# Optimization experiments

Hardware: AMD Instinct MI355X
Metric: run time of the kernel (lower is better)

The kernel has to match this reference:

```python
import jax, jax.numpy as jnp
import numpy as np

WH, WW = 7, 7
N = WH * WW
HEADS = 12
HEAD_DIM = 16
EMBED = 384
INNER = HEADS * HEAD_DIM
NW = 64
B_ = 2048
SCALE = HEAD_DIM ** -0.5


def _relative_position_index():
    ch, cw = np.meshgrid(np.arange(WH), np.arange(WW), indexing='ij')
    coords = np.stack([ch.ravel(), cw.ravel()])              # [2, N]
    rel = coords[:, :, None] - coords[:, None, :]             # [2, N, N]
    rel = rel.transpose(1, 2, 0)
    rel[:, :, 0] += WH - 1
    rel[:, :, 1] += WW - 1
    rel[:, :, 0] *= 2 * WW - 1
    return jnp.asarray(rel.sum(-1), dtype=jnp.int32)          # [N, N]


def setup_inputs() -> dict:
    key = jax.random.key(0)
    ks = jax.random.split(key, 8)
    s_in = EMBED ** -0.5
    s_inner = INNER ** -0.5
    x = jax.random.normal(ks[0], (B_, N, EMBED), jnp.float32)
    # Swin shift mask: 0 or -100 per window pair
    mbits = jax.random.bernoulli(ks[1], 0.2, (NW, N, N))
    mask = jnp.where(mbits, jnp.float32(-100.0), jnp.float32(0.0))
    return {
        'x': x,
        'mask': mask,
        'Wq': jax.random.normal(ks[2], (EMBED, INNER), jnp.float32) * s_in,
        'bq': jnp.zeros((INNER,), jnp.float32),
        'Wk': jax.random.normal(ks[3], (EMBED, INNER), jnp.float32) * s_in,
        'bk': jnp.zeros((INNER,), jnp.float32),
        'Wv': jax.random.normal(ks[4], (EMBED, INNER), jnp.float32) * s_in,
        'bv': jnp.zeros((INNER,), jnp.float32),
        'Wp': jax.random.normal(ks[5], (INNER, EMBED), jnp.float32) * s_inner,
        'bp': jnp.zeros((EMBED,), jnp.float32),
        'bias_table': jax.random.normal(ks[6], ((2 * WH - 1) * (2 * WW - 1), HEADS), jnp.float32) * 0.02,
        'rel_idx': _relative_position_index(),
    }


def reference(x, mask, Wq, bq, Wk, bk, Wv, bv, Wp, bp, bias_table, rel_idx):
    B, n, _ = x.shape
    q = (x @ Wq + bq).reshape(B, n, HEADS, HEAD_DIM)
    k = (x @ Wk + bk).reshape(B, n, HEADS, HEAD_DIM)
    v = (x @ Wv + bv).reshape(B, n, HEADS, HEAD_DIM)
    attn = jnp.einsum('bnhd,bmhd->bhnm', q * SCALE, k)        # [B, H, N, N]
    bias = bias_table[rel_idx]                                 # [N, N, H]
    attn = attn + jnp.transpose(bias, (2, 0, 1))[None]
    nW = mask.shape[0]
    attn = attn.reshape(B // nW, nW, HEADS, n, n) + mask[None, :, None]
    attn = jax.nn.softmax(attn.reshape(B, HEADS, n, n), axis=-1)
    out = jnp.einsum('bhnm,bmhd->bnhd', attn, v).reshape(B, n, INNER)
    return out @ Wp + bp
```

## Files before the change

kernel.cpp:

```cpp
#include <hip/hip_runtime.h>


typedef __attribute__((ext_vector_type(8))) short  bf8;
typedef __attribute__((ext_vector_type(4))) short  bf4;
typedef __attribute__((ext_vector_type(4))) float  f4;

#define L2E 1.4426950408889634f

union VU { unsigned u[2]; bf4 v; };

__device__ __forceinline__ short f2b(float f) {
  unsigned u = __builtin_bit_cast(unsigned, f);
  unsigned r = u + 0x7fffu + ((u >> 16) & 1u);
  return (short)(r >> 16);
}
__device__ __forceinline__ unsigned pk2(float lo, float hi) {
  return (unsigned)(unsigned short)f2b(lo) | ((unsigned)(unsigned short)f2b(hi) << 16);
}
__device__ __forceinline__ bf4 pkbf4(f4 v) {
  VU r; r.u[0] = pk2(v[0], v[1]); r.u[1] = pk2(v[2], v[3]);
  return r.v;
}
__device__ __forceinline__ float b2f(unsigned short b) {
  return __builtin_bit_cast(float, (unsigned)b << 16);
}
__device__ __forceinline__ float ex2(float x) {
#if __has_builtin(__builtin_amdgcn_exp2f)
  return __builtin_amdgcn_exp2f(x);
#else
  float r; asm("v_exp_f32 %0, %1" : "=v"(r) : "v"(x)); return r;
#endif
}
__device__ __forceinline__ f4 mfma16(bf4 a, bf4 b, f4 c) {
#if __has_builtin(__builtin_amdgcn_mfma_f32_16x16x16bf16_1k)
  return __builtin_amdgcn_mfma_f32_16x16x16bf16_1k(a, b, c, 0, 0, 0);
#else
  f4 d;
  asm("v_mfma_f32_16x16x16_bf16 %0, %1, %2, %3" : "=v"(d) : "v"(a), "v"(b), "v"(c));
  return d;
#endif
}

__global__ void wa_prep(const float* __restrict__ Wq, const float* __restrict__ Wk,
                        const float* __restrict__ Wv, const float* __restrict__ Wp,
                        const float* __restrict__ btab, const int* __restrict__ ridx,
                        const float* __restrict__ mask,
                        short* __restrict__ wt, short* __restrict__ wpt,
                        unsigned short* __restrict__ biasS, unsigned short* __restrict__ maskS) {
  int id = blockIdx.x * 256 + threadIdx.x;
  const int NWT = 576 * 384, NWP = 384 * 192, NBS = 12 * 64 * 64, NMS = 64 * 64 * 64;
  if (id < NWT) {
    int row = id / 384, k = id - row * 384;
    int kind = row / 192, cc = row - kind * 192;
    const float* W = (kind == 0) ? Wq : (kind == 1 ? Wk : Wv);
    float v = W[k * 192 + cc];
    if (kind == 0) v *= 0.25f * L2E;
    wt[id] = f2b(v);
  } else if ((id -= NWT) < NWP) {
    int n = id / 192, k = id - n * 192;
    wpt[id] = f2b(Wp[k * 384 + n]);
  } else if ((id -= NWP) < NBS) {
    int h = id >> 12, rem = id & 4095;
    int n = rem >> 6, cc = rem & 63;
    int m = (cc & 3) * 16 + (cc >> 2);
    float v;
    if (n >= 49)      v = -14427.0f;
    else if (m >= 49) v = 0.0f;
    else              v = btab[ridx[m * 49 + n] * 12 + h] * L2E;
    biasS[id] = (unsigned short)f2b(v);
  } else if ((id -= NBS) < NMS) {
    int win = id >> 12, rem = id & 4095;
    int n = rem >> 6, cc = rem & 63;
    int m = (cc & 3) * 16 + (cc >> 2);
    float v = (m < 49 && n < 49) ? mask[win * 2401 + m * 49 + n] * L2E : 0.f;
    maskS[id] = (unsigned short)f2b(v);
  }
}

struct __align__(16) Smem {
  union U {
    short xs[64][392];
    struct QK { short qs[64][200]; short ks[64][200]; } qk;
  } u;
};

__global__ __launch_bounds__(256, 2)
void wa_main(const float* __restrict__ x,
             const float* __restrict__ bq, const float* __restrict__ bk,
             const float* __restrict__ bv, const float* __restrict__ bp,
             const short* __restrict__ wt, const short* __restrict__ wpt,
             const unsigned short* __restrict__ biasS, const unsigned short* __restrict__ maskS,
             float* __restrict__ out) {
  __shared__ Smem sm;
  const int tid = threadIdx.x;
  const int w   = tid >> 6;
  const int lid = tid & 63;
  const int g   = lid >> 4;
  const int c   = lid & 15;
  const int blk = blockIdx.x;
  const int mwin = (blk & 63) << 12;

  {
    const float* xw = x + (size_t)blk * 18816;
    f4 xv[18];
#pragma unroll
    for (int it = 0; it < 18; it++) {
      int i = tid + it * 256;
      xv[it] = *(const f4*)(xw + (i / 96) * 384 + (i % 96) * 4);
    }
    const int iT = tid + 18 * 256;
    f4 xt = {0.f, 0.f, 0.f, 0.f};
    if (iT < 4704) xt = *(const f4*)(xw + (iT / 96) * 384 + (iT % 96) * 4);
#pragma unroll
    for (int it = 0; it < 18; it++) {
      int i = tid + it * 256;
      *(bf4*)&sm.u.xs[i / 96][(i % 96) * 4] = pkbf4(xv[it]);
    }
    if (iT < 4704) *(bf4*)&sm.u.xs[iT / 96][(iT % 96) * 4] = pkbf4(xt);
    const bf8 zz = {0,0,0,0,0,0,0,0};
#pragma unroll
    for (int it = 0; it < 3; it++) {
      int i = tid + it * 256;
      if (i < 735) { int row = 49 + i / 49, c8 = (i % 49) * 8; *(bf8*)&sm.u.xs[row][c8] = zz; }
    }
  }
  __syncthreads();

  f4 acc[4][9];
#pragma unroll
  for (int mt = 0; mt < 4; mt++)
#pragma unroll
    for (int i = 0; i < 9; i++) acc[mt][i] = (f4){0.f, 0.f, 0.f, 0.f};
  int rowb[9];
#pragma unroll
  for (int i = 0; i < 9; i++) {
    int kind = i / 3, hh = 3 * w + i % 3;
    rowb[i] = (kind * 192 + hh * 16 + c) * 384;
  }
#pragma unroll 3
  for (int ks = 0; ks < 12; ks++) {
    const int k0 = ks * 32 + g * 8;
    bf8 a[4], b[9];
#pragma unroll
    for (int mt = 0; mt < 4; mt++) a[mt] = *(const bf8*)&sm.u.xs[mt * 16 + c][k0];
#pragma unroll
    for (int i = 0; i < 9; i++) b[i] = *(const bf8*)(wt + rowb[i] + k0);
#pragma unroll
    for (int mt = 0; mt < 4; mt++)
#pragma unroll
      for (int i = 0; i < 9; i++)
        acc[mt][i] = __builtin_amdgcn_mfma_f32_16x16x32_bf16(a[mt], b[i], acc[mt][i], 0, 0, 0);
  }
  __syncthreads();

  unsigned vpk[3][4][2];
#pragma unroll
  for (int i = 0; i < 9; i++) {
    const int kind = i / 3, hh = 3 * w + i % 3;
    const int col = hh * 16 + c;
    const float bb = (kind == 0) ? (0.25f * L2E) * bq[col] : (kind == 1 ? bk[col] : bv[col]);
#pragma unroll
    for (int mt = 0; mt < 4; mt++) {
      unsigned w0 = pk2(acc[mt][i][0] + bb, acc[mt][i][1] + bb);
      unsigned w1 = pk2(acc[mt][i][2] + bb, acc[mt][i][3] + bb);
      if (kind == 2) {
        vpk[i - 6][mt][0] = w0;
        vpk[i - 6][mt][1] = w1;
      } else {
        short* dst = (kind == 0) ? &sm.u.qk.qs[0][0] : &sm.u.qk.ks[0][0];
        dst[(mt * 16 + g * 4 + 0) * 200 + col] = (short)(w0 & 0xFFFFu);
        dst[(mt * 16 + g * 4 + 1) * 200 + col] = (short)(w0 >> 16);
        dst[(mt * 16 + g * 4 + 2) * 200 + col] = (short)(w1 & 0xFFFFu);
        dst[(mt * 16 + g * 4 + 3) * 200 + col] = (short)(w1 >> 16);
      }
    }
  }
  asm volatile("" ::: "memory");

  const f4 z4 = {0.f, 0.f, 0.f, 0.f};
#pragma unroll
  for (int t = 0; t < 3; t++) {
    const int h  = 3 * w + t;
    const int hb = h * 16;
    bf4 afr[4], bfr[4];
#pragma unroll
    for (int nt = 0; nt < 4; nt++)
      afr[nt] = *(const bf4*)&sm.u.qk.ks[nt * 16 + c][hb + g * 4];
#pragma unroll
    for (int mt = 0; mt < 4; mt++)
      bfr[mt] = *(const bf4*)&sm.u.qk.qs[mt * 16 + c][hb + g * 4];
    f4 s[4][4];
#pragma unroll
    for (int nt = 0; nt < 4; nt++)
#pragma unroll
      for (int mt = 0; mt < 4; mt++)
        s[nt][mt] = mfma16(afr[nt], bfr[mt], z4);
    const unsigned short* bsH = biasS + (h << 12);
#pragma unroll
    for (int nt = 0; nt < 4; nt++)
#pragma unroll
      for (int r = 0; r < 4; r++) {
        const int n = nt * 16 + g * 4 + r;
        bf4 b4 = *(const bf4*)&bsH[n * 64 + c * 4];
        bf4 m4 = *(const bf4*)&maskS[mwin + n * 64 + c * 4];
#pragma unroll
        for (int mt = 0; mt < 4; mt++)
          s[nt][mt][r] += b2f((unsigned short)b4[mt]) + b2f((unsigned short)m4[mt]);
      }
    float rin[4];
#pragma unroll
    for (int mt = 0; mt < 4; mt++) {
      float mx = -3e38f;
#pragma unroll
      for (int nt = 0; nt < 4; nt++)
#pragma unroll
        for (int r = 0; r < 4; r++) mx = fmaxf(mx, s[nt][mt][r]);
      mx = fmaxf(mx, __shfl_xor(mx, 16, 64));
      mx = fmaxf(mx, __shfl_xor(mx, 32, 64));
      float sum = 0.f;
#pragma unroll
      for (int nt = 0; nt < 4; nt++)
#pragma unroll
        for (int r = 0; r < 4; r++) {
          float p = ex2(s[nt][mt][r] - mx);
          s[nt][mt][r] = p;
          sum += p;
        }
      sum += __shfl_xor(sum, 16, 64);
      sum += __shfl_xor(sum, 32, 64);
      rin[mt] = 1.f / sum;
    }
    unsigned ppk[4][4][2];
#pragma unroll
    for (int nt = 0; nt < 4; nt++)
#pragma unroll
      for (int mt = 0; mt < 4; mt++) {
        ppk[nt][mt][0] = pk2(s[nt][mt][0], s[nt][mt][1]);
        ppk[nt][mt][1] = pk2(s[nt][mt][2], s[nt][mt][3]);
      }
    f4 o[4];
#pragma unroll
    for (int mt = 0; mt < 4; mt++) o[mt] = z4;
#pragma unroll
    for (int kt = 0; kt < 4; kt++) {
      VU vu; vu.u[0] = vpk[t][kt][0]; vu.u[1] = vpk[t][kt][1];
#pragma unroll
      for (int mt = 0; mt < 4; mt++) {
        VU pu; pu.u[0] = ppk[kt][mt][0]; pu.u[1] = ppk[kt][mt][1];
        o[mt] = mfma16(vu.v, pu.v, o[mt]);
      }
    }
#pragma unroll
    for (int mt = 0; mt < 4; mt++) {
      f4 ov = o[mt] * rin[mt];
      *(bf4*)&sm.u.qk.qs[mt * 16 + c][hb + g * 4] = pkbf4(ov);
    }
    asm volatile("" ::: "memory");
  }

  bf8 wb0[6];
#pragma unroll
  for (int jt = 0; jt < 6; jt++)
    wb0[jt] = *(const bf8*)(wpt + (w * 96 + jt * 16 + c) * 192 + g * 8);
  __syncthreads();

  f4 acc3[6][4];
#pragma unroll
  for (int jt = 0; jt < 6; jt++)
#pragma unroll
    for (int mt = 0; mt < 4; mt++) acc3[jt][mt] = z4;
  {
    const int k0 = g * 8;
    bf8 ao[4];
#pragma unroll
    for (int mt = 0; mt < 4; mt++) ao[mt] = *(const bf8*)&sm.u.qk.qs[mt * 16 + c][k0];
#pragma unroll
    for (int jt = 0; jt < 6; jt++)
#pragma unroll
      for (int mt = 0; mt < 4; mt++)
        acc3[jt][mt] = __builtin_amdgcn_mfma_f32_16x16x32_bf16(wb0[jt], ao[mt], acc3[jt][mt], 0, 0, 0);
  }
#pragma unroll 2
  for (int ks3 = 1; ks3 < 6; ks3++) {
    const int k0 = ks3 * 32 + g * 8;
    bf8 ao[4], wb[6];
#pragma unroll
    for (int mt = 0; mt < 4; mt++) ao[mt] = *(const bf8*)&sm.u.qk.qs[mt * 16 + c][k0];
#pragma unroll
    for (int jt = 0; jt < 6; jt++)
      wb[jt] = *(const bf8*)(wpt + (w * 96 + jt * 16 + c) * 192 + k0);
#pragma unroll
    for (int jt = 0; jt < 6; jt++)
#pragma unroll
      for (int mt = 0; mt < 4; mt++)
        acc3[jt][mt] = __builtin_amdgcn_mfma_f32_16x16x32_bf16(wb[jt], ao[mt], acc3[jt][mt], 0, 0, 0);
  }
  float* ow = out + (size_t)blk * 18816;
#pragma unroll
  for (int jt = 0; jt < 6; jt++) {
    const int colb = w * 96 + jt * 16 + g * 4;
    const f4 bp4 = *(const f4*)&bp[colb];
#pragma unroll
    for (int mt = 0; mt < 4; mt++) {
      const int m = mt * 16 + c;
      if (m < 49) {
        f4 v = acc3[jt][mt] + bp4;
        *(f4*)&ow[m * 384 + colb] = v;
      }
    }
  }
}

extern "C" void kernel_launch(void* const* d_in, const int* in_sizes, int n_in,
                              void* d_out, int out_size, void* d_ws, size_t ws_size,
                              hipStream_t stream) {
  const float* x    = (const float*)d_in[0];
  const float* mask = (const float*)d_in[1];
  const float* Wq   = (const float*)d_in[2];
  const float* bq   = (const float*)d_in[3];
  const float* Wk   = (const float*)d_in[4];
  const float* bk   = (const float*)d_in[5];
  const float* Wv   = (const float*)d_in[6];
  const float* bv   = (const float*)d_in[7];
  const float* Wp   = (const float*)d_in[8];
  const float* bp   = (const float*)d_in[9];
  const float* btab = (const float*)d_in[10];
  const int*   ridx = (const int*)d_in[11];
  float* out = (float*)d_out;

  char* ws = (char*)d_ws;
  short* wt            = (short*)ws;
  short* wpt           = (short*)(ws + 442368);
  unsigned short* biasS = (unsigned short*)(ws + 589824);
  unsigned short* maskS = (unsigned short*)(ws + 688128);

  wa_prep<<<dim3(2368), dim3(256), 0, stream>>>(Wq, Wk, Wv, Wp, btab, ridx, mask,
                                                wt, wpt, biasS, maskS);
  wa_main<<<dim3(2048), dim3(256), 0, stream>>>(x, bq, bk, bv, bp, wt, wpt, biasS, maskS, out);
}
```

Measured before the change: 224.1 us.

## Stage V through shared memory and disable unrolling to cut register pressure

V projections are no longer held in registers across the attention loop; they are written transposed to a new shared array and reloaded per head. Several loops drop full unrolling, and the peeled first Wp prefetch step is folded back into the projection loop. The aim is to lower VGPR usage, possibly to reach the requested two blocks per CU, at the cost of extra LDS traffic, about 26KB more shared memory per block, and less instruction-level overlap.

```diff
diff --git a/kernel.cpp b/kernel.cpp
--- a/kernel.cpp
+++ b/kernel.cpp
@@ -82,6 +82,7 @@
     short xs[64][392];
     struct QK { short qs[64][200]; short ks[64][200]; } qk;
   } u;
+  short vts[192][68];
 };
 
 __global__ __launch_bounds__(256, 2)
@@ -153,19 +154,19 @@
   }
   __syncthreads();
 
-  unsigned vpk[3][4][2];
-#pragma unroll
+#pragma unroll 1
   for (int i = 0; i < 9; i++) {
-    const int kind = i / 3, hh = 3 * w + i % 3;
-    const int col = hh * 16 + c;
-    const float bb = (kind == 0) ? (0.25f * L2E) * bq[col] : (kind == 1 ? bk[col] : bv[col]);
+    const int kind = i / 3;
+    const int col = (3 * w + i % 3) * 16 + c;
+    const float* bptr = (kind == 0) ? bq : (kind == 1 ? bk : bv);
+    const float bb = bptr[col] * ((kind == 0) ? 0.25f * L2E : 1.0f);
 #pragma unroll
     for (int mt = 0; mt < 4; mt++) {
       unsigned w0 = pk2(acc[mt][i][0] + bb, acc[mt][i][1] + bb);
       unsigned w1 = pk2(acc[mt][i][2] + bb, acc[mt][i][3] + bb);
       if (kind == 2) {
-        vpk[i - 6][mt][0] = w0;
-        vpk[i - 6][mt][1] = w1;
+        VU vv; vv.u[0] = w0; vv.u[1] = w1;
+        *(bf4*)&sm.vts[col][mt * 16 + g * 4] = vv.v;
       } else {
         short* dst = (kind == 0) ? &sm.u.qk.qs[0][0] : &sm.u.qk.ks[0][0];
         dst[(mt * 16 + g * 4 + 0) * 200 + col] = (short)(w0 & 0xFFFFu);
@@ -178,7 +179,7 @@
   asm volatile("" ::: "memory");
 
   const f4 z4 = {0.f, 0.f, 0.f, 0.f};
-#pragma unroll
+#pragma unroll 1
   for (int t = 0; t < 3; t++) {
     const int h  = 3 * w + t;
     const int hb = h * 16;
@@ -243,11 +244,11 @@
     for (int mt = 0; mt < 4; mt++) o[mt] = z4;
 #pragma unroll
     for (int kt = 0; kt < 4; kt++) {
-      VU vu; vu.u[0] = vpk[t][kt][0]; vu.u[1] = vpk[t][kt][1];
+      bf4 va = *(const bf4*)&sm.vts[hb + c][kt * 16 + g * 4];
 #pragma unroll
       for (int mt = 0; mt < 4; mt++) {
         VU pu; pu.u[0] = ppk[kt][mt][0]; pu.u[1] = ppk[kt][mt][1];
-        o[mt] = mfma16(vu.v, pu.v, o[mt]);
+        o[mt] = mfma16(va, pu.v, o[mt]);
       }
     }
 #pragma unroll
@@ -257,31 +258,15 @@
     }
     asm volatile("" ::: "memory");
   }
-
-  bf8 wb0[6];
+  __syncthreads();
+
+  f4 acc3[6][4];
 #pragma unroll
   for (int jt = 0; jt < 6; jt++)
-    wb0[jt] = *(const bf8*)(wpt + (w * 96 + jt * 16 + c) * 192 + g * 8);
-  __syncthreads();
-
-  f4 acc3[6][4];
-#pragma unroll
-  for (int jt = 0; jt < 6; jt++)
 #pragma unroll
     for (int mt = 0; mt < 4; mt++) acc3[jt][mt] = z4;
-  {
-    const int k0 = g * 8;
-    bf8 ao[4];
-#pragma unroll
-    for (int mt = 0; mt < 4; mt++) ao[mt] = *(const bf8*)&sm.u.qk.qs[mt * 16 + c][k0];
-#pragma unroll
-    for (int jt = 0; jt < 6; jt++)
-#pragma unroll
-      for (int mt = 0; mt < 4; mt++)
-        acc3[jt][mt] = __builtin_amdgcn_mfma_f32_16x16x32_bf16(wb0[jt], ao[mt], acc3[jt][mt], 0, 0, 0);
-  }
-#pragma unroll 2
-  for (int ks3 = 1; ks3 < 6; ks3++) {
+#pragma unroll 1
+  for (int ks3 = 0; ks3 < 6; ks3++) {
     const int k0 = ks3 * 32 + g * 8;
     bf8 ao[4], wb[6];
 #pragma unroll
```

Result: slower. 358.4 us (+59.9%).
